# Kernel optimization log

Measured on AMD Instinct MI355X. Metric: run time of the kernel, lower is better.

## Reference

```python
import jax, jax.numpy as jnp
import numpy as np

N = 8192
IN_DIM = 256
HIDDEN = 128


def setup_inputs() -> dict:
    key = jax.random.key(0)
    k1, k2 = jax.random.split(key)
    X = jax.random.normal(k1, (N, IN_DIM), dtype=jnp.float32)
    # nn.Linear(in_dim, hidden, bias=False): weight [hidden, in_dim]
    W = jax.random.normal(k2, (HIDDEN, IN_DIM), dtype=jnp.float32) * (1.0 / np.sqrt(IN_DIM))
    return {"X": X, "W": W}


def reference(X, W):
    # Z = X @ W.T : [N, hidden]
    Z = jnp.einsum('ni,hi->nh', X, W)
    # Dense similarity graph: ReLU(Z Z^T), row-normalized
    A = jax.nn.relu(jnp.einsum('nh,mh->nm', Z, Z))  # [N, N]
    A = A / (A.sum(axis=-1, keepdims=True) + 1e-6)
    out = jnp.einsum('nm,mh->nh', A, Z)  # [N, hidden]
    return (out, A)
```

## Files before the change

kernel.cpp:

```cpp
#include <hip/hip_runtime.h>


#define NR 8192
#define KD 256
#define HD 128

typedef short v8s __attribute__((ext_vector_type(8)));
typedef float v4f __attribute__((ext_vector_type(4)));

static __device__ __forceinline__ ushort f2bf(float f) {
    union { float f; unsigned u; } c; c.f = f;
    unsigned u = c.u;
    u += 0x7fffu + ((u >> 16) & 1u);
    return (ushort)(u >> 16);
}
static __device__ __forceinline__ float bf2f(ushort b) {
    union { unsigned u; float f; } c; c.u = ((unsigned)b) << 16; return c.f;
}
static __device__ __forceinline__ unsigned pk2(float a, float b) {
    union { float f; unsigned u; } x, y; x.f = a; y.f = b;
    unsigned ua = x.u + 0x7fffu + ((x.u >> 16) & 1u);
    unsigned ub = y.u + 0x7fffu + ((y.u >> 16) & 1u);
    return (ua >> 16) | (ub & 0xffff0000u);
}

__global__ __launch_bounds__(256) void k_z(const float* __restrict__ X,
                                           const float* __restrict__ W,
                                           ushort* __restrict__ Zb,
                                           ushort* __restrict__ ZbT) {
    __shared__ ushort Xhi[32][264];
    __shared__ ushort Xlo[32][264];
    int tid = threadIdx.x, lane = tid & 63, wave = tid >> 6;
    int lm = lane & 15, lq = lane >> 4;
    int n0 = blockIdx.x * 32;
    int hbase = wave * 32;
    v8s Whi[2][8], Wlo[2][8];
#pragma unroll
    for (int hi = 0; hi < 2; ++hi) {
        const float* wp = W + (hbase + hi * 16 + lm) * KD + lq * 8;
#pragma unroll
        for (int ks = 0; ks < 8; ++ks) {
            float4 w0 = *(const float4*)(wp + ks * 32);
            float4 w1 = *(const float4*)(wp + ks * 32 + 4);
            float wv[8] = {w0.x, w0.y, w0.z, w0.w, w1.x, w1.y, w1.z, w1.w};
#pragma unroll
            for (int j = 0; j < 8; ++j) {
                ushort h = f2bf(wv[j]);
                Whi[hi][ks][j] = (short)h;
                Wlo[hi][ks][j] = (short)f2bf(wv[j] - bf2f(h));
            }
        }
    }
#pragma unroll
    for (int t = 0; t < 8; ++t) {
        int idx = tid + t * 256;
        int r = idx >> 6, c4 = (idx & 63) * 4;
        float4 x = *(const float4*)(X + (size_t)(n0 + r) * KD + c4);
        ushort h0 = f2bf(x.x), h1 = f2bf(x.y), h2 = f2bf(x.z), h3 = f2bf(x.w);
        unsigned a = ((unsigned)h0) | ((unsigned)h1 << 16);
        unsigned b = ((unsigned)h2) | ((unsigned)h3 << 16);
        unsigned c = ((unsigned)f2bf(x.x - bf2f(h0))) | ((unsigned)f2bf(x.y - bf2f(h1)) << 16);
        unsigned d = ((unsigned)f2bf(x.z - bf2f(h2))) | ((unsigned)f2bf(x.w - bf2f(h3)) << 16);
        *(uint2*)&Xhi[r][c4] = make_uint2(a, b);
        *(uint2*)&Xlo[r][c4] = make_uint2(c, d);
    }
    __syncthreads();
#pragma unroll
    for (int ni = 0; ni < 2; ++ni) {
        v8s Ah[8], Al[8];
#pragma unroll
        for (int ks = 0; ks < 8; ++ks) {
            Ah[ks] = *(const v8s*)&Xhi[ni * 16 + lm][ks * 32 + lq * 8];
            Al[ks] = *(const v8s*)&Xlo[ni * 16 + lm][ks * 32 + lq * 8];
        }
        v4f acc[2] = {{0.f, 0.f, 0.f, 0.f}, {0.f, 0.f, 0.f, 0.f}};
#pragma unroll
        for (int ks = 0; ks < 8; ++ks)
#pragma unroll
            for (int hi = 0; hi < 2; ++hi) {
                acc[hi] = __builtin_amdgcn_mfma_f32_16x16x32_bf16(Ah[ks], Whi[hi][ks], acc[hi], 0, 0, 0);
                acc[hi] = __builtin_amdgcn_mfma_f32_16x16x32_bf16(Ah[ks], Wlo[hi][ks], acc[hi], 0, 0, 0);
                acc[hi] = __builtin_amdgcn_mfma_f32_16x16x32_bf16(Al[ks], Whi[hi][ks], acc[hi], 0, 0, 0);
            }
#pragma unroll
        for (int hi = 0; hi < 2; ++hi) {
            int h = hbase + hi * 16 + lm;
            int nb = n0 + ni * 16 + lq * 4;
            ushort b0 = f2bf(acc[hi][0]), b1 = f2bf(acc[hi][1]);
            ushort b2 = f2bf(acc[hi][2]), b3 = f2bf(acc[hi][3]);
            Zb[(size_t)(nb + 0) * HD + h] = b0;
            Zb[(size_t)(nb + 1) * HD + h] = b1;
            Zb[(size_t)(nb + 2) * HD + h] = b2;
            Zb[(size_t)(nb + 3) * HD + h] = b3;
            *(uint2*)&ZbT[(size_t)h * NR + nb] =
                make_uint2(((unsigned)b0) | ((unsigned)b1 << 16), ((unsigned)b2) | ((unsigned)b3 << 16));
        }
    }
}

__global__ __launch_bounds__(256) void k_rowsum(const ushort* __restrict__ Zb,
                                                float* __restrict__ rowsum) {
    __shared__ ushort ZR[128][136];
    __shared__ ushort ZC[128][136];
    int tid = threadIdx.x, lane = tid & 63, wave = tid >> 6;
    int lm = lane & 15, lq = lane >> 4;
    int rb = blockIdx.x >> 3, cs = blockIdx.x & 7;
    int row0 = rb * 128, cstart = cs * 1024;
#pragma unroll
    for (int t = 0; t < 8; ++t) {
        int idx = tid + t * 256;
        int r = idx >> 4, c8 = (idx & 15) * 8;
        *(uint4*)&ZR[r][c8] = *(const uint4*)(Zb + (size_t)(row0 + r) * HD + c8);
    }
    __syncthreads();
    int wr2 = wave >> 1, wc2 = wave & 1;
    v8s Bfr[4][4];
#pragma unroll
    for (int ri = 0; ri < 4; ++ri)
#pragma unroll
        for (int ks = 0; ks < 4; ++ks)
            Bfr[ri][ks] = *(const v8s*)&ZR[wr2 * 64 + ri * 16 + lm][ks * 32 + lq * 8];
    float rs[4] = {0.f, 0.f, 0.f, 0.f};
    for (int it = 0; it < 8; ++it) {
        int c0 = cstart + it * 128;
        __syncthreads();
#pragma unroll
        for (int t = 0; t < 8; ++t) {
            int idx = tid + t * 256;
            int r = idx >> 4, c8 = (idx & 15) * 8;
            *(uint4*)&ZC[r][c8] = *(const uint4*)(Zb + (size_t)(c0 + r) * HD + c8);
        }
        __syncthreads();
#pragma unroll
        for (int ci = 0; ci < 4; ++ci) {
            v8s Af[4];
#pragma unroll
            for (int ks = 0; ks < 4; ++ks)
                Af[ks] = *(const v8s*)&ZC[wc2 * 64 + ci * 16 + lm][ks * 32 + lq * 8];
            v4f acc[4] = {{0.f,0.f,0.f,0.f},{0.f,0.f,0.f,0.f},{0.f,0.f,0.f,0.f},{0.f,0.f,0.f,0.f}};
#pragma unroll
            for (int ks = 0; ks < 4; ++ks)
#pragma unroll
                for (int ri = 0; ri < 4; ++ri)
                    acc[ri] = __builtin_amdgcn_mfma_f32_16x16x32_bf16(Af[ks], Bfr[ri][ks], acc[ri], 0, 0, 0);
#pragma unroll
            for (int ri = 0; ri < 4; ++ri)
                rs[ri] += fmaxf(acc[ri][0], 0.f) + fmaxf(acc[ri][1], 0.f) +
                          fmaxf(acc[ri][2], 0.f) + fmaxf(acc[ri][3], 0.f);
        }
    }
#pragma unroll
    for (int ri = 0; ri < 4; ++ri) {
        float v = rs[ri];
        v += __shfl_xor(v, 16, 64);
        v += __shfl_xor(v, 32, 64);
        if (lq == 0) atomicAdd(&rowsum[row0 + wr2 * 64 + ri * 16 + lm], v);
    }
}

__global__ __launch_bounds__(256) void k_main(const ushort* __restrict__ Zb,
                                              const ushort* __restrict__ ZbT,
                                              const float* __restrict__ rowsum,
                                              float* __restrict__ outp,
                                              float* __restrict__ Ap) {
    __shared__ ushort ZR[64][136];
    __shared__ ushort ZC[64][136];
    __shared__ ushort ZCT[128][72];
    __shared__ ushort PT[64][72];
    int tid = threadIdx.x, lane = tid & 63, wave = tid >> 6;
    int lm = lane & 15, lq = lane >> 4;
    int rb = blockIdx.x >> 2, cs = blockIdx.x & 3;
    int row0 = rb * 64, colb = cs * 2048;
#pragma unroll
    for (int t = 0; t < 4; ++t) {
        int idx = tid + t * 256;
        int r = idx >> 4, c8 = (idx & 15) * 8;
        *(uint4*)&ZR[r][c8] = *(const uint4*)(Zb + (size_t)(row0 + r) * HD + c8);
    }
    __syncthreads();
    int wr2 = wave >> 1, wc2 = wave & 1;
    v8s Bfr[2][4];
#pragma unroll
    for (int ri = 0; ri < 2; ++ri)
#pragma unroll
        for (int ks = 0; ks < 4; ++ks)
            Bfr[ri][ks] = *(const v8s*)&ZR[wr2 * 32 + ri * 16 + lm][ks * 32 + lq * 8];
    float rsv[2];
#pragma unroll
    for (int ri = 0; ri < 2; ++ri)
        rsv[ri] = 1.0f / (rowsum[row0 + wr2 * 32 + ri * 16 + lm] + 1e-6f);
    v4f U[2][4];
#pragma unroll
    for (int ri = 0; ri < 2; ++ri)
#pragma unroll
        for (int hi = 0; hi < 4; ++hi) U[ri][hi] = (v4f){0.f, 0.f, 0.f, 0.f};

    for (int it = 0; it < 32; ++it) {
        int c0 = colb + it * 64;
        __syncthreads();
#pragma unroll
        for (int t = 0; t < 4; ++t) {
            int idx = tid + t * 256;
            int r = idx >> 4, c8 = (idx & 15) * 8;
            *(uint4*)&ZC[r][c8] = *(const uint4*)(Zb + (size_t)(c0 + r) * HD + c8);
        }
#pragma unroll
        for (int t = 0; t < 4; ++t) {
            int idx = tid + t * 256;
            int hh = idx >> 3, cc8 = (idx & 7) * 8;
            *(uint4*)&ZCT[hh][cc8] = *(const uint4*)(ZbT + (size_t)hh * NR + c0 + cc8);
        }
        __syncthreads();
#pragma unroll
        for (int ci = 0; ci < 2; ++ci) {
            v8s Af[4];
#pragma unroll
            for (int ks = 0; ks < 4; ++ks)
                Af[ks] = *(const v8s*)&ZC[wc2 * 32 + ci * 16 + lm][ks * 32 + lq * 8];
            v4f S0 = {0.f, 0.f, 0.f, 0.f}, S1 = {0.f, 0.f, 0.f, 0.f};
#pragma unroll
            for (int ks = 0; ks < 4; ++ks) {
                S0 = __builtin_amdgcn_mfma_f32_16x16x32_bf16(Af[ks], Bfr[0][ks], S0, 0, 0, 0);
                S1 = __builtin_amdgcn_mfma_f32_16x16x32_bf16(Af[ks], Bfr[1][ks], S1, 0, 0, 0);
            }
            int cb = wc2 * 32 + ci * 16 + lq * 4;
            {
                int r = wr2 * 32 + lm;
                v4f av;
                av[0] = fmaxf(S0[0], 0.f) * rsv[0]; av[1] = fmaxf(S0[1], 0.f) * rsv[0];
                av[2] = fmaxf(S0[2], 0.f) * rsv[0]; av[3] = fmaxf(S0[3], 0.f) * rsv[0];
                __builtin_nontemporal_store(av, (v4f*)(Ap + (size_t)(row0 + r) * NR + c0 + cb));
                *(uint2*)&PT[r][cb] = make_uint2(pk2(av[0], av[1]), pk2(av[2], av[3]));
            }
            {
                int r = wr2 * 32 + 16 + lm;
                v4f av;
                av[0] = fmaxf(S1[0], 0.f) * rsv[1]; av[1] = fmaxf(S1[1], 0.f) * rsv[1];
                av[2] = fmaxf(S1[2], 0.f) * rsv[1]; av[3] = fmaxf(S1[3], 0.f) * rsv[1];
                __builtin_nontemporal_store(av, (v4f*)(Ap + (size_t)(row0 + r) * NR + c0 + cb));
                *(uint2*)&PT[r][cb] = make_uint2(pk2(av[0], av[1]), pk2(av[2], av[3]));
            }
        }
        __syncthreads();
#pragma unroll
        for (int ks = 0; ks < 2; ++ks) {
            v8s P0 = *(const v8s*)&PT[wr2 * 32 + lm][ks * 32 + lq * 8];
            v8s P1 = *(const v8s*)&PT[wr2 * 32 + 16 + lm][ks * 32 + lq * 8];
#pragma unroll
            for (int hi = 0; hi < 4; ++hi) {
                v8s Bz = *(const v8s*)&ZCT[wc2 * 64 + hi * 16 + lm][ks * 32 + lq * 8];
                U[0][hi] = __builtin_amdgcn_mfma_f32_16x16x32_bf16(P0, Bz, U[0][hi], 0, 0, 0);
                U[1][hi] = __builtin_amdgcn_mfma_f32_16x16x32_bf16(P1, Bz, U[1][hi], 0, 0, 0);
            }
        }
    }
#pragma unroll
    for (int ri = 0; ri < 2; ++ri)
#pragma unroll
        for (int hi = 0; hi < 4; ++hi)
#pragma unroll
            for (int j = 0; j < 4; ++j)
                atomicAdd(&outp[(size_t)(row0 + wr2 * 32 + ri * 16 + lq * 4 + j) * HD +
                                wc2 * 64 + hi * 16 + lm],
                          U[ri][hi][j]);
}

extern "C" void kernel_launch(void* const* d_in, const int* in_sizes, int n_in,
                              void* d_out, int out_size, void* d_ws, size_t ws_size,
                              hipStream_t stream) {
    (void)in_sizes; (void)n_in; (void)out_size; (void)ws_size;
    const float* X = (const float*)d_in[0];
    const float* W = (const float*)d_in[1];
    float* outp = (float*)d_out;
    float* Ap = outp + (size_t)NR * HD;
    char* ws = (char*)d_ws;
    ushort* Zb = (ushort*)ws;
    ushort* ZbT = (ushort*)(ws + (size_t)NR * HD * 2);
    float* rowsum = (float*)(ws + (size_t)NR * HD * 4);

    (void)hipMemsetAsync(outp, 0, (size_t)NR * HD * sizeof(float), stream);
    (void)hipMemsetAsync(rowsum, 0, NR * sizeof(float), stream);
    k_z<<<dim3(NR / 32), dim3(256), 0, stream>>>(X, W, Zb, ZbT);
    k_rowsum<<<dim3(512), dim3(256), 0, stream>>>(Zb, rowsum);
    k_main<<<dim3(512), dim3(256), 0, stream>>>(Zb, ZbT, rowsum, outp, Ap);
}
```

Before: 367.7 us.

## Load MFMA operands directly from global memory and double-buffer the P tile

Removes the shared-memory staging of the Z row, column and transposed tiles in both the rowsum and main kernels. Each wave now loads its MFMA operand fragments straight from global memory, which drops most of the __syncthreads per iteration. The P tile becomes double-buffered so only one barrier per iteration is needed, and the nontemporal A stores are moved after that barrier. In exchange, operands that several waves share are fetched repeatedly through L1/L2, and the per-lane 16-byte global loads may be less coalesced than the old cooperative loads.

Result: slower. 427.3 us (+16.2%).

```diff
diff --git a/kernel.cpp b/kernel.cpp
--- a/kernel.cpp
+++ b/kernel.cpp
@@ -100,43 +100,26 @@
 
 __global__ __launch_bounds__(256) void k_rowsum(const ushort* __restrict__ Zb,
                                                 float* __restrict__ rowsum) {
-    __shared__ ushort ZR[128][136];
-    __shared__ ushort ZC[128][136];
     int tid = threadIdx.x, lane = tid & 63, wave = tid >> 6;
     int lm = lane & 15, lq = lane >> 4;
     int rb = blockIdx.x >> 3, cs = blockIdx.x & 7;
     int row0 = rb * 128, cstart = cs * 1024;
-#pragma unroll
-    for (int t = 0; t < 8; ++t) {
-        int idx = tid + t * 256;
-        int r = idx >> 4, c8 = (idx & 15) * 8;
-        *(uint4*)&ZR[r][c8] = *(const uint4*)(Zb + (size_t)(row0 + r) * HD + c8);
-    }
-    __syncthreads();
     int wr2 = wave >> 1, wc2 = wave & 1;
     v8s Bfr[4][4];
 #pragma unroll
     for (int ri = 0; ri < 4; ++ri)
 #pragma unroll
         for (int ks = 0; ks < 4; ++ks)
-            Bfr[ri][ks] = *(const v8s*)&ZR[wr2 * 64 + ri * 16 + lm][ks * 32 + lq * 8];
+            Bfr[ri][ks] = *(const v8s*)(Zb + (size_t)(row0 + wr2 * 64 + ri * 16 + lm) * HD + ks * 32 + lq * 8);
     float rs[4] = {0.f, 0.f, 0.f, 0.f};
     for (int it = 0; it < 8; ++it) {
-        int c0 = cstart + it * 128;
-        __syncthreads();
-#pragma unroll
-        for (int t = 0; t < 8; ++t) {
-            int idx = tid + t * 256;
-            int r = idx >> 4, c8 = (idx & 15) * 8;
-            *(uint4*)&ZC[r][c8] = *(const uint4*)(Zb + (size_t)(c0 + r) * HD + c8);
-        }
-        __syncthreads();
+        int c0 = cstart + it * 128 + wc2 * 64;
 #pragma unroll
         for (int ci = 0; ci < 4; ++ci) {
             v8s Af[4];
 #pragma unroll
             for (int ks = 0; ks < 4; ++ks)
-                Af[ks] = *(const v8s*)&ZC[wc2 * 64 + ci * 16 + lm][ks * 32 + lq * 8];
+                Af[ks] = *(const v8s*)(Zb + (size_t)(c0 + ci * 16 + lm) * HD + ks * 32 + lq * 8);
             v4f acc[4] = {{0.f,0.f,0.f,0.f},{0.f,0.f,0.f,0.f},{0.f,0.f,0.f,0.f},{0.f,0.f,0.f,0.f}};
 #pragma unroll
             for (int ks = 0; ks < 4; ++ks)
@@ -163,28 +146,18 @@
                                               const float* __restrict__ rowsum,
                                               float* __restrict__ outp,
                                               float* __restrict__ Ap) {
-    __shared__ ushort ZR[64][136];
-    __shared__ ushort ZC[64][136];
-    __shared__ ushort ZCT[128][72];
-    __shared__ ushort PT[64][72];
+    __shared__ ushort PT[2][64][72];
     int tid = threadIdx.x, lane = tid & 63, wave = tid >> 6;
     int lm = lane & 15, lq = lane >> 4;
     int rb = blockIdx.x >> 2, cs = blockIdx.x & 3;
     int row0 = rb * 64, colb = cs * 2048;
-#pragma unroll
-    for (int t = 0; t < 4; ++t) {
-        int idx = tid + t * 256;
-        int r = idx >> 4, c8 = (idx & 15) * 8;
-        *(uint4*)&ZR[r][c8] = *(const uint4*)(Zb + (size_t)(row0 + r) * HD + c8);
-    }
-    __syncthreads();
     int wr2 = wave >> 1, wc2 = wave & 1;
     v8s Bfr[2][4];
 #pragma unroll
     for (int ri = 0; ri < 2; ++ri)
 #pragma unroll
         for (int ks = 0; ks < 4; ++ks)
-            Bfr[ri][ks] = *(const v8s*)&ZR[wr2 * 32 + ri * 16 + lm][ks * 32 + lq * 8];
+            Bfr[ri][ks] = *(const v8s*)(Zb + (size_t)(row0 + wr2 * 32 + ri * 16 + lm) * HD + ks * 32 + lq * 8);
     float rsv[2];
 #pragma unroll
     for (int ri = 0; ri < 2; ++ri)
@@ -197,26 +170,14 @@
 
     for (int it = 0; it < 32; ++it) {
         int c0 = colb + it * 64;
-        __syncthreads();
-#pragma unroll
-        for (int t = 0; t < 4; ++t) {
-            int idx = tid + t * 256;
-            int r = idx >> 4, c8 = (idx & 15) * 8;
-            *(uint4*)&ZC[r][c8] = *(const uint4*)(Zb + (size_t)(c0 + r) * HD + c8);
-        }
-#pragma unroll
-        for (int t = 0; t < 4; ++t) {
-            int idx = tid + t * 256;
-            int hh = idx >> 3, cc8 = (idx & 7) * 8;
-            *(uint4*)&ZCT[hh][cc8] = *(const uint4*)(ZbT + (size_t)hh * NR + c0 + cc8);
-        }
-        __syncthreads();
+        int b = it & 1;
+        v4f av[2][2];
 #pragma unroll
         for (int ci = 0; ci < 2; ++ci) {
             v8s Af[4];
 #pragma unroll
             for (int ks = 0; ks < 4; ++ks)
-                Af[ks] = *(const v8s*)&ZC[wc2 * 32 + ci * 16 + lm][ks * 32 + lq * 8];
+                Af[ks] = *(const v8s*)(Zb + (size_t)(c0 + wc2 * 32 + ci * 16 + lm) * HD + ks * 32 + lq * 8);
             v4f S0 = {0.f, 0.f, 0.f, 0.f}, S1 = {0.f, 0.f, 0.f, 0.f};
 #pragma unroll
             for (int ks = 0; ks < 4; ++ks) {
@@ -224,31 +185,29 @@
                 S1 = __builtin_amdgcn_mfma_f32_16x16x32_bf16(Af[ks], Bfr[1][ks], S1, 0, 0, 0);
             }
             int cb = wc2 * 32 + ci * 16 + lq * 4;
-            {
-                int r = wr2 * 32 + lm;
-                v4f av;
-                av[0] = fmaxf(S0[0], 0.f) * rsv[0]; av[1] = fmaxf(S0[1], 0.f) * rsv[0];
-                av[2] = fmaxf(S0[2], 0.f) * rsv[0]; av[3] = fmaxf(S0[3], 0.f) * rsv[0];
-                __builtin_nontemporal_store(av, (v4f*)(Ap + (size_t)(row0 + r) * NR + c0 + cb));
-                *(uint2*)&PT[r][cb] = make_uint2(pk2(av[0], av[1]), pk2(av[2], av[3]));
-            }
-            {
-                int r = wr2 * 32 + 16 + lm;
-                v4f av;
-                av[0] = fmaxf(S1[0], 0.f) * rsv[1]; av[1] = fmaxf(S1[1], 0.f) * rsv[1];
-                av[2] = fmaxf(S1[2], 0.f) * rsv[1]; av[3] = fmaxf(S1[3], 0.f) * rsv[1];
-                __builtin_nontemporal_store(av, (v4f*)(Ap + (size_t)(row0 + r) * NR + c0 + cb));
-                *(uint2*)&PT[r][cb] = make_uint2(pk2(av[0], av[1]), pk2(av[2], av[3]));
-            }
+            v4f a0, a1;
+            a0[0] = fmaxf(S0[0], 0.f) * rsv[0]; a0[1] = fmaxf(S0[1], 0.f) * rsv[0];
+            a0[2] = fmaxf(S0[2], 0.f) * rsv[0]; a0[3] = fmaxf(S0[3], 0.f) * rsv[0];
+            a1[0] = fmaxf(S1[0], 0.f) * rsv[1]; a1[1] = fmaxf(S1[1], 0.f) * rsv[1];
+            a1[2] = fmaxf(S1[2], 0.f) * rsv[1]; a1[3] = fmaxf(S1[3], 0.f) * rsv[1];
+            av[ci][0] = a0; av[ci][1] = a1;
+            *(uint2*)&PT[b][wr2 * 32 + lm][cb] = make_uint2(pk2(a0[0], a0[1]), pk2(a0[2], a0[3]));
+            *(uint2*)&PT[b][wr2 * 32 + 16 + lm][cb] = make_uint2(pk2(a1[0], a1[1]), pk2(a1[2], a1[3]));
         }
         __syncthreads();
 #pragma unroll
+        for (int ci = 0; ci < 2; ++ci) {
+            int cb = wc2 * 32 + ci * 16 + lq * 4;
+            __builtin_nontemporal_store(av[ci][0], (v4f*)(Ap + (size_t)(row0 + wr2 * 32 + lm) * NR + c0 + cb));
+            __builtin_nontemporal_store(av[ci][1], (v4f*)(Ap + (size_t)(row0 + wr2 * 32 + 16 + lm) * NR + c0 + cb));
+        }
+#pragma unroll
         for (int ks = 0; ks < 2; ++ks) {
-            v8s P0 = *(const v8s*)&PT[wr2 * 32 + lm][ks * 32 + lq * 8];
-            v8s P1 = *(const v8s*)&PT[wr2 * 32 + 16 + lm][ks * 32 + lq * 8];
+            v8s P0 = *(const v8s*)&PT[b][wr2 * 32 + lm][ks * 32 + lq * 8];
+            v8s P1 = *(const v8s*)&PT[b][wr2 * 32 + 16 + lm][ks * 32 + lq * 8];
 #pragma unroll
             for (int hi = 0; hi < 4; ++hi) {
-                v8s Bz = *(const v8s*)&ZCT[wc2 * 64 + hi * 16 + lm][ks * 32 + lq * 8];
+                v8s Bz = *(const v8s*)(ZbT + (size_t)(wc2 * 64 + hi * 16 + lm) * NR + c0 + ks * 32 + lq * 8);
                 U[0][hi] = __builtin_amdgcn_mfma_f32_16x16x32_bf16(P0, Bz, U[0][hi], 0, 0, 0);
                 U[1][hi] = __builtin_amdgcn_mfma_f32_16x16x32_bf16(P1, Bz, U[1][hi], 0, 0, 0);
             }
```
